# Optimization experiments

Measured on AMD Instinct MI355X. Metric: run time of the kernel, lower is better.

## Reference

```python
import jax, jax.numpy as jnp
import numpy as np

B, N, A, O, D, Q, H = 64, 4, 1024, 128, 256, 256, 128
NEG_INF = -1e30


def setup_inputs() -> dict:
    key = jax.random.key(0)
    ks = jax.random.split(key, 8)
    q = jax.random.normal(ks[0], (B, N, 1, Q), dtype=jnp.float32)
    att1 = jax.random.uniform(ks[1], (B, N, A, O), dtype=jnp.float32)
    obj_reps = jax.random.normal(ks[2], (B, O, D), dtype=jnp.float32)
    tags_attention = jax.random.randint(ks[3], (B, N, A), 0, 2, dtype=jnp.int32)
    W1 = jax.random.normal(ks[4], (D + Q, H), dtype=jnp.float32) / np.sqrt(D + Q)
    b1 = jnp.zeros((H,), dtype=jnp.float32)
    W2 = jax.random.normal(ks[5], (H, 1), dtype=jnp.float32) / np.sqrt(H)
    b2 = jnp.zeros((1,), dtype=jnp.float32)
    return {"q": q, "att1": att1, "obj_reps": obj_reps,
            "tags_attention": tags_attention,
            "W1": W1, "b1": b1, "W2": W2, "b2": b2, "t": 1}


def reference(q, att1, obj_reps, tags_attention, W1, b1, W2, b2, t):
    # v: [B,N,A,D] = att1 [B,N,A,O] @ obj_reps [B,O,D]
    v = jnp.einsum('bnao,bod->bnad', att1, obj_reps)
    # q broadcast over token dim A, concat -> [B,N,A,D+Q]
    q_proj = jnp.broadcast_to(q, v.shape[:3] + (q.shape[-1],))
    vq = jnp.concatenate([v, q_proj], axis=-1)
    # FCNet: Linear + ReLU (dropout is identity at inference)
    joint_repr = jax.nn.relu(vq @ W1 + b1)          # [B,N,A,H]
    logits = (joint_repr @ W2 + b2)[..., 0]          # [B,N,A]
    # temperature-scaled masked softmax over tokens
    masked = jnp.where(tags_attention > 0, logits / t, NEG_INF)
    att2 = jax.nn.softmax(masked, axis=-1)           # [B,N,A]
    # attention_last: [B,N,O] = att2 [B,N,1,A] @ att1 [B,N,A,O]
    return jnp.einsum('bna,bnao->bno', att2, att1)
```

## Files before the change

kernel.cpp:

```cpp
#include <hip/hip_runtime.h>
#include <math.h>

#define Bc 64
#define Nc 4
#define Ac 1024
#define Oc 128
#define Dc 256
#define Qc 256
#define Hc 128
#define BN (Bc*Nc)

using f4     = __attribute__((ext_vector_type(4))) float;
using f32x4  = __attribute__((ext_vector_type(4))) float;
using short8 = __attribute__((ext_vector_type(8))) short;
using us4    = __attribute__((ext_vector_type(4))) unsigned short;

__device__ inline float decode_t(const void* p) {
    int i = *(const int*)p;
    if (i >= 1 && i <= 1000000) return (float)i;
    return __int_as_float(i);
}

__device__ inline unsigned short bf16_rne(float x) {
    unsigned u = __builtin_bit_cast(unsigned, x);
    u += 0x7FFFu + ((u >> 16) & 1u);
    return (unsigned short)(u >> 16);
}

__device__ inline void split_bf16(float x, unsigned short& hi, unsigned short& lo) {
    unsigned u = __builtin_bit_cast(unsigned, x);
    hi = (unsigned short)(u >> 16);
    float hif = __builtin_bit_cast(float, u & 0xFFFF0000u);
    float lof = x - hif;
    lo = (unsigned short)(__builtin_bit_cast(unsigned, lof) >> 16);
}

__global__ __launch_bounds__(256) void prep_M_kernel(
    const float* __restrict__ obj, const float* __restrict__ W1,
    unsigned short* __restrict__ Mt_hi, unsigned short* __restrict__ Mt_lo)
{
    __shared__ float w_s[32][36];
    __shared__ float obj_sT[32][68];

    const int t  = threadIdx.x;
    const int tx = t & 15;
    const int ty = t >> 4;
    const int h0 = blockIdx.x * 32;
    const int o0 = blockIdx.y * 64;
    const int b  = blockIdx.z;
    const int r8 = t >> 3, c8 = t & 7;

    const float* objb = obj + ((size_t)b * Oc + o0) * Dc;

    float acc[2][4];
    #pragma unroll
    for (int i = 0; i < 2; i++)
        #pragma unroll
        for (int j = 0; j < 4; j++) acc[i][j] = 0.f;

    f4 wv  = *(const f4*)(W1 + (size_t)r8 * Hc + h0 + c8 * 4);
    f4 ov0 = *(const f4*)(objb + (size_t)r8 * Dc + c8 * 4);
    f4 ov1 = *(const f4*)(objb + (size_t)(r8 + 32) * Dc + c8 * 4);

    for (int ko = 0; ko < 8; ++ko) {
        *(f4*)&w_s[r8][c8 * 4] = wv;
        obj_sT[c8 * 4 + 0][r8] = ov0[0];
        obj_sT[c8 * 4 + 1][r8] = ov0[1];
        obj_sT[c8 * 4 + 2][r8] = ov0[2];
        obj_sT[c8 * 4 + 3][r8] = ov0[3];
        obj_sT[c8 * 4 + 0][r8 + 32] = ov1[0];
        obj_sT[c8 * 4 + 1][r8 + 32] = ov1[1];
        obj_sT[c8 * 4 + 2][r8 + 32] = ov1[2];
        obj_sT[c8 * 4 + 3][r8 + 32] = ov1[3];
        __syncthreads();
        if (ko < 7) {
            wv  = *(const f4*)(W1 + (size_t)((ko + 1) * 32 + r8) * Hc + h0 + c8 * 4);
            ov0 = *(const f4*)(objb + (size_t)r8 * Dc + (ko + 1) * 32 + c8 * 4);
            ov1 = *(const f4*)(objb + (size_t)(r8 + 32) * Dc + (ko + 1) * 32 + c8 * 4);
        }
        #pragma unroll 4
        for (int k = 0; k < 32; k++) {
            float a0 = w_s[k][ty * 2];
            float a1 = w_s[k][ty * 2 + 1];
            f4 bv = *(const f4*)&obj_sT[k][tx * 4];
            #pragma unroll
            for (int j = 0; j < 4; j++) {
                acc[0][j] += a0 * bv[j];
                acc[1][j] += a1 * bv[j];
            }
        }
        __syncthreads();
    }

    #pragma unroll
    for (int i = 0; i < 2; i++) {
        us4 hi, lo;
        #pragma unroll
        for (int j = 0; j < 4; j++) {
            unsigned short h16, l16;
            split_bf16(acc[i][j], h16, l16);
            hi[j] = h16; lo[j] = l16;
        }
        size_t ofs = ((size_t)b * Hc + h0 + ty * 2 + i) * Oc + o0 + tx * 4;
        *(us4*)(Mt_hi + ofs) = hi;
        *(us4*)(Mt_lo + ofs) = lo;
    }
}

__global__ __launch_bounds__(512) void prep_qb_kernel(
    const float* __restrict__ q, const float* __restrict__ W1,
    const float* __restrict__ b1, float* __restrict__ qb)
{
    __shared__ float qs[256];
    __shared__ float red[4][128];
    const int t = threadIdx.x;
    const int bn = blockIdx.x;

    if (t < 256) qs[t] = q[bn * Qc + t];
    __syncthreads();

    const int h = t & 127, kq = t >> 7;
    float acc = 0.f;
    const float* w = W1 + (size_t)(Dc + kq * 64) * Hc + h;
    #pragma unroll 8
    for (int d = 0; d < 64; ++d)
        acc += qs[kq * 64 + d] * w[(size_t)d * Hc];
    red[kq][h] = acc;
    __syncthreads();

    if (t < 128)
        qb[bn * Hc + t] = b1[t] + red[0][t] + red[1][t] + red[2][t] + red[3][t];
}

__global__ __launch_bounds__(1024, 4) void main_kernel(
    const float* __restrict__ att1, const int* __restrict__ tags,
    const unsigned short* __restrict__ Mt_hi, const unsigned short* __restrict__ Mt_lo,
    const float* __restrict__ qb, const float* __restrict__ W2,
    const float* __restrict__ b2, const void* __restrict__ tptr,
    float* __restrict__ out)
{
    __shared__ unsigned short A_s[2][128][136];
    __shared__ float part2[128][9];
    __shared__ float part3[8][132];
    __shared__ float e_s[128];
    __shared__ float qb_s[128], w2_s[128];
    __shared__ float zfin[2];

    const int t    = threadIdx.x;
    const int wave = t >> 6;
    const int lane = t & 63;
    const int l15  = lane & 15;
    const int quad = lane >> 4;
    const int bn = blockIdx.x;
    const int b  = bn >> 2;
    const int rowg = (wave >> 3) * 64;
    const int hw   = (wave & 7) * 16;

    const float* att_bn = att1 + (size_t)bn * Ac * Oc;

    f4 sv[4];
    #pragma unroll
    for (int s = 0; s < 4; s++) {
        int idx = t + 1024 * s;
        sv[s] = *(const f4*)(att_bn + (size_t)idx * 4);
    }

    const size_t brow = ((size_t)b * Hc + hw + l15) * Oc;
    short8 Bh[4], Bl[4];
    #pragma unroll
    for (int ks = 0; ks < 4; ks++) {
        const int ko = ks * 32 + quad * 8;
        Bh[ks] = *(const short8*)(Mt_hi + brow + ko);
        Bl[ks] = *(const short8*)(Mt_lo + brow + ko);
    }

    if (t < 128) { qb_s[t] = qb[bn * Hc + t]; w2_s[t] = W2[t]; }
    int tg_cur = (t < 128) ? tags[(size_t)bn * Ac + t] : 0;
    const float b2v  = b2[0];
    const float tval = decode_t(tptr);

    float z_reg = 0.f, out_reg = 0.f;

    for (int tile = 0; tile < 8; ++tile) {
        const int buf = tile & 1;
        const float* tile_ptr = att_bn + (size_t)tile * 128 * Oc;

        #pragma unroll
        for (int s = 0; s < 4; s++) {
            int idx = t + 1024 * s;
            int r = idx >> 5, c4 = idx & 31;
            us4 h4;
            #pragma unroll
            for (int j = 0; j < 4; j++) h4[j] = bf16_rne(sv[s][j]);
            *(us4*)&A_s[buf][r][c4 * 4] = h4;
        }
        __syncthreads();

        int tg_next = 0;
        if (tile < 7) {
            const float* np = att_bn + (size_t)(tile + 1) * 128 * Oc;
            #pragma unroll
            for (int s = 0; s < 4; s++) {
                int idx = t + 1024 * s;
                sv[s] = *(const f4*)(np + (size_t)idx * 4);
            }
            if (t < 128) tg_next = tags[(size_t)bn * Ac + (tile + 1) * 128 + t];
        }

        f32x4 acc[4];
        #pragma unroll
        for (int i = 0; i < 4; i++) acc[i] = (f32x4)(0.f);
        #pragma unroll
        for (int ks = 0; ks < 4; ks++) {
            const int ko = ks * 32 + quad * 8;
            #pragma unroll
            for (int i = 0; i < 4; i++) {
                short8 ah = *(const short8*)&A_s[buf][rowg + i * 16 + l15][ko];
                acc[i] = __builtin_amdgcn_mfma_f32_16x16x32_bf16(ah, Bh[ks], acc[i], 0, 0, 0);
                acc[i] = __builtin_amdgcn_mfma_f32_16x16x32_bf16(ah, Bl[ks], acc[i], 0, 0, 0);
            }
        }

        {
            const float qbv = qb_s[hw + l15], w2v = w2_s[hw + l15];
            float p[4][4];
            #pragma unroll
            for (int i = 0; i < 4; i++)
                #pragma unroll
                for (int r = 0; r < 4; r++) {
                    float v = acc[i][r] + qbv;
                    v = v > 0.f ? v : 0.f;
                    p[i][r] = v * w2v;
                }
            #pragma unroll
            for (int m = 1; m <= 8; m <<= 1)
                #pragma unroll
                for (int i = 0; i < 4; i++)
                    #pragma unroll
                    for (int r = 0; r < 4; r++)
                        p[i][r] += __shfl_xor(p[i][r], m);
            if (l15 == 0) {
                #pragma unroll
                for (int i = 0; i < 4; i++)
                    #pragma unroll
                    for (int r = 0; r < 4; r++)
                        part2[rowg + i * 16 + quad * 4 + r][wave & 7] = p[i][r];
            }
        }
        __syncthreads();

        if (t < 128) {
            float sum = b2v;
            #pragma unroll
            for (int x = 0; x < 8; x++) sum += part2[t][x];
            float logit = sum / tval;
            float e = (tg_cur > 0) ? __expf(logit) : 0.f;
            e_s[t] = e;
            z_reg += e;
        }
        __syncthreads();

        {
            const int o  = t & 127;
            const int g  = t >> 7;
            const float* ab = tile_ptr + (size_t)(g * 16) * Oc + o;
            float accum = 0.f;
            #pragma unroll
            for (int a = 0; a < 16; a++)
                accum += e_s[g * 16 + a] * ab[(size_t)a * Oc];
            part3[g][o] = accum;
        }
        __syncthreads();

        if (t < 128) {
            float s = 0.f;
            #pragma unroll
            for (int g = 0; g < 8; g++) s += part3[g][t];
            out_reg += s;
        }
        tg_cur = tg_next;
    }

    __syncthreads();
    if (t < 128) {
        float z = z_reg;
        #pragma unroll
        for (int off = 32; off > 0; off >>= 1) z += __shfl_down(z, off);
        if (lane == 0) zfin[wave] = z;
    }
    __syncthreads();
    if (t < 128) {
        float Z = zfin[0] + zfin[1];
        out[(size_t)bn * Oc + t] = out_reg / Z;
    }
}

extern "C" void kernel_launch(void* const* d_in, const int* in_sizes, int n_in,
                              void* d_out, int out_size, void* d_ws, size_t ws_size,
                              hipStream_t stream)
{
    (void)in_sizes; (void)n_in; (void)out_size; (void)ws_size;

    const float* q    = (const float*)d_in[0];
    const float* att1 = (const float*)d_in[1];
    const float* obj  = (const float*)d_in[2];
    const int*   tags = (const int*)d_in[3];
    const float* W1   = (const float*)d_in[4];
    const float* b1   = (const float*)d_in[5];
    const float* W2   = (const float*)d_in[6];
    const float* b2   = (const float*)d_in[7];
    const void*  tptr = d_in[8];
    float* out = (float*)d_out;

    char* wsb = (char*)d_ws;
    unsigned short* Mt_hi = (unsigned short*)wsb;
    unsigned short* Mt_lo = (unsigned short*)(wsb + (size_t)2*1024*1024);
    float* qbuf = (float*)(wsb + (size_t)4*1024*1024);

    prep_M_kernel<<<dim3(4, 2, Bc), 256, 0, stream>>>(obj, W1, Mt_hi, Mt_lo);
    prep_qb_kernel<<<dim3(BN), 512, 0, stream>>>(q, W1, b1, qbuf);
    main_kernel<<<dim3(BN), 1024, 0, stream>>>(att1, tags, Mt_hi, Mt_lo,
                                               qbuf, W2, b2, tptr, out);
}
```

Baseline: 248.7 us.

## Switch hidden-layer GEMM to 32x32x16 MFMA with transposed operand roles

Replaces the 16x16x32 bf16 MFMA tiling with 32x32x16 MFMA. The weight matrix (hi/lo split) becomes the register-resident A operand, the token tile in LDS becomes B, and each wave covers a 32x32 output block. The ReLU/W2 reduction now accumulates within each lane across the 16 accumulator registers and needs only one cross-half shuffle. This cuts the shuffle work and the partial sums per row from 8 to 4. It also halves the LDS reads per MFMA, at the cost of more registers held for the weights.

```diff
diff --git a/kernel.cpp b/kernel.cpp
--- a/kernel.cpp
+++ b/kernel.cpp
@@ -11,7 +11,7 @@
 #define BN (Bc*Nc)
 
 using f4     = __attribute__((ext_vector_type(4))) float;
-using f32x4  = __attribute__((ext_vector_type(4))) float;
+using f32x16 = __attribute__((ext_vector_type(16))) float;
 using short8 = __attribute__((ext_vector_type(8))) short;
 using us4    = __attribute__((ext_vector_type(4))) unsigned short;
 
@@ -140,21 +140,21 @@
     float* __restrict__ out)
 {
     __shared__ unsigned short A_s[2][128][136];
-    __shared__ float part2[128][9];
+    __shared__ float part2[128][5];
     __shared__ float part3[8][132];
     __shared__ float e_s[128];
-    __shared__ float qb_s[128], w2_s[128];
+    __shared__ float2 qw_s[128];
     __shared__ float zfin[2];
 
     const int t    = threadIdx.x;
     const int wave = t >> 6;
     const int lane = t & 63;
-    const int l15  = lane & 15;
-    const int quad = lane >> 4;
+    const int l31  = lane & 31;
+    const int half = lane >> 5;
+    const int ag   = wave & 3;
+    const int hg   = wave >> 2;
     const int bn = blockIdx.x;
     const int b  = bn >> 2;
-    const int rowg = (wave >> 3) * 64;
-    const int hw   = (wave & 7) * 16;
 
     const float* att_bn = att1 + (size_t)bn * Ac * Oc;
 
@@ -165,16 +165,18 @@
         sv[s] = *(const f4*)(att_bn + (size_t)idx * 4);
     }
 
-    const size_t brow = ((size_t)b * Hc + hw + l15) * Oc;
-    short8 Bh[4], Bl[4];
+    const size_t arow = ((size_t)b * Hc + hg * 32 + l31) * Oc + half * 8;
+    short8 Ah[8], Al[8];
     #pragma unroll
-    for (int ks = 0; ks < 4; ks++) {
-        const int ko = ks * 32 + quad * 8;
-        Bh[ks] = *(const short8*)(Mt_hi + brow + ko);
-        Bl[ks] = *(const short8*)(Mt_lo + brow + ko);
-    }
-
-    if (t < 128) { qb_s[t] = qb[bn * Hc + t]; w2_s[t] = W2[t]; }
+    for (int ks = 0; ks < 8; ks++) {
+        Ah[ks] = *(const short8*)(Mt_hi + arow + ks * 16);
+        Al[ks] = *(const short8*)(Mt_lo + arow + ks * 16);
+    }
+
+    if (t < 128) {
+        float2 qw; qw.x = qb[bn * Hc + t]; qw.y = W2[t];
+        qw_s[t] = qw;
+    }
     int tg_cur = (t < 128) ? tags[(size_t)bn * Ac + t] : 0;
     const float b2v  = b2[0];
     const float tval = decode_t(tptr);
@@ -207,52 +209,29 @@
             if (t < 128) tg_next = tags[(size_t)bn * Ac + (tile + 1) * 128 + t];
         }
 
-        f32x4 acc[4];
-        #pragma unroll
-        for (int i = 0; i < 4; i++) acc[i] = (f32x4)(0.f);
-        #pragma unroll
-        for (int ks = 0; ks < 4; ks++) {
-            const int ko = ks * 32 + quad * 8;
-            #pragma unroll
-            for (int i = 0; i < 4; i++) {
-                short8 ah = *(const short8*)&A_s[buf][rowg + i * 16 + l15][ko];
-                acc[i] = __builtin_amdgcn_mfma_f32_16x16x32_bf16(ah, Bh[ks], acc[i], 0, 0, 0);
-                acc[i] = __builtin_amdgcn_mfma_f32_16x16x32_bf16(ah, Bl[ks], acc[i], 0, 0, 0);
-            }
-        }
-
-        {
-            const float qbv = qb_s[hw + l15], w2v = w2_s[hw + l15];
-            float p[4][4];
-            #pragma unroll
-            for (int i = 0; i < 4; i++)
-                #pragma unroll
-                for (int r = 0; r < 4; r++) {
-                    float v = acc[i][r] + qbv;
-                    v = v > 0.f ? v : 0.f;
-                    p[i][r] = v * w2v;
-                }
-            #pragma unroll
-            for (int m = 1; m <= 8; m <<= 1)
-                #pragma unroll
-                for (int i = 0; i < 4; i++)
-                    #pragma unroll
-                    for (int r = 0; r < 4; r++)
-                        p[i][r] += __shfl_xor(p[i][r], m);
-            if (l15 == 0) {
-                #pragma unroll
-                for (int i = 0; i < 4; i++)
-                    #pragma unroll
-                    for (int r = 0; r < 4; r++)
-                        part2[rowg + i * 16 + quad * 4 + r][wave & 7] = p[i][r];
-            }
-        }
+        f32x16 acc = (f32x16)(0.f);
+        #pragma unroll
+        for (int ks = 0; ks < 8; ks++) {
+            short8 bv = *(const short8*)&A_s[buf][ag * 32 + l31][ks * 16 + half * 8];
+            acc = __builtin_amdgcn_mfma_f32_32x32x16_bf16(Ah[ks], bv, acc, 0, 0, 0);
+            acc = __builtin_amdgcn_mfma_f32_32x32x16_bf16(Al[ks], bv, acc, 0, 0, 0);
+        }
+
+        float p = 0.f;
+        #pragma unroll
+        for (int reg = 0; reg < 16; reg++) {
+            int h = hg * 32 + (reg & 3) + 8 * (reg >> 2) + 4 * half;
+            float2 qw = qw_s[h];
+            float v = acc[reg] + qw.x;
+            v = v > 0.f ? v : 0.f;
+            p += v * qw.y;
+        }
+        p += __shfl_xor(p, 32);
+        if (half == 0) part2[ag * 32 + l31][hg] = p;
         __syncthreads();
 
         if (t < 128) {
-            float sum = b2v;
-            #pragma unroll
-            for (int x = 0; x < 8; x++) sum += part2[t][x];
+            float sum = part2[t][0] + part2[t][1] + part2[t][2] + part2[t][3] + b2v;
             float logit = sum / tval;
             float e = (tg_cur > 0) ? __expf(logit) : 0.f;
             e_s[t] = e;
@@ -261,8 +240,8 @@
         __syncthreads();
 
         {
-            const int o  = t & 127;
-            const int g  = t >> 7;
+            const int o = t & 127;
+            const int g = t >> 7;
             const float* ab = tile_ptr + (size_t)(g * 16) * Oc + o;
             float accum = 0.f;
             #pragma unroll
```

New measurement: 252.9 us. No clear change (+1.7%).
